# Kernel optimization log

Measured on AMD Instinct MI355X. Metric: run time of the kernel, lower is better.

Reference implementation:

```python
import jax, jax.numpy as jnp
import numpy as np

B, V, R, C, UNITS = 16, 10000, 8, 64, 64


def setup_inputs() -> dict:
    key = jax.random.key(0)
    k1, k2, k3 = jax.random.split(key, 3)
    nodes = jax.random.normal(k1, (B, V, C), dtype=jnp.float32)
    mapping = jax.random.randint(k2, (B, V, R), -1, V, dtype=jnp.int32)
    kernel = jax.random.normal(k3, (R * C, UNITS), dtype=jnp.float32) * 0.02
    bias = jnp.zeros((UNITS,), dtype=jnp.float32)
    return {"nodes": nodes, "mapping": mapping, "kernel": kernel, "bias": bias}


def reference(nodes, mapping, kernel, bias):
    # nodes: [B, V, C], mapping: [B, V, R] int32 in [-1, V)
    b, v, r = mapping.shape
    c = nodes.shape[-1]
    idx = jnp.clip(mapping, 0, v - 1)                       # safe gather indices
    batch_idx = jnp.arange(b, dtype=jnp.int32)[:, None, None]
    gathered = nodes[batch_idx, idx]                        # [B, V, R, C]
    valid = (mapping >= 0)[..., None]                       # -1 -> zero (scatter_nd default)
    cols = jnp.where(valid, gathered, jnp.zeros((), nodes.dtype))
    cols = cols.reshape(b, v, r * c)                        # [B, V, R*C]
    out = jnp.einsum("bvf,fu->bvu", cols, kernel) + bias    # dense + bias
    return jax.nn.relu(out)
```

## Files before the change

### kernel.cpp

```cpp
#include <hip/hip_runtime.h>
#include <hip/hip_fp16.h>


#define Bn 16
#define Vn 10000
#define Rn 8
#define Cn 64
#define Un 64

#define LOSCALE 2048.0f
#define LOINV   (1.0f/2048.0f)

typedef _Float16      f16x8   __attribute__((ext_vector_type(8)));
typedef __fp16        fp16x2  __attribute__((ext_vector_type(2)));
typedef float         f32x16  __attribute__((ext_vector_type(16)));
typedef unsigned int  u32x4   __attribute__((ext_vector_type(4)));
typedef unsigned short us8    __attribute__((ext_vector_type(8)));

__device__ __forceinline__ unsigned short f16b(_Float16 h) {
    return __builtin_bit_cast(unsigned short, h);
}

__device__ __forceinline__ unsigned int cvt2w(float a0, float a1) {
    const fp16x2 p = __builtin_amdgcn_cvt_pkrtz(a0, a1);
    return __builtin_bit_cast(unsigned int, p);
}
__device__ __forceinline__ _Float16 loh(unsigned int w) {
    return __builtin_bit_cast(_Float16, (unsigned short)(w & 0xffff));
}
__device__ __forceinline__ _Float16 hih(unsigned int w) {
    return __builtin_bit_cast(_Float16, (unsigned short)(w >> 16));
}

#define LDS_LO 65536

__global__ __launch_bounds__(512, 2)
void graphconv_kernel(const float* __restrict__ nodes,
                      const int* __restrict__ mapping,
                      const float* __restrict__ kern,
                      const float* __restrict__ bias,
                      float* __restrict__ out) {
    extern __shared__ unsigned char lds[];
    const int tid  = threadIdx.x;
    const int lane = tid & 63;
    const int w    = tid >> 6;
    const int g    = blockIdx.x;
    const int b    = g & 15;
    const int v0   = (g >> 4) << 8;

    const int row = lane & 31;
    const int grp = lane >> 5;
    const int v   = v0 + w * 32 + row;
    const bool vok = v < Vn;

    int4 m03 = make_int4(-1, -1, -1, -1), m47 = make_int4(-1, -1, -1, -1);
    if (vok) {
        const int4* mp4 = (const int4*)(mapping + ((size_t)b * Vn + v) * Rn);
        m03 = mp4[0];
        m47 = mp4[1];
    }

    #pragma unroll
    for (int it = 0; it < 8; ++it) {
        const int gg = it * 512 + tid;
        const int f  = gg >> 6;
        const int l  = gg & 63;
        const int nt = f >> 5;
        const int kt = f & 31;
        const int n  = nt * 32 + (l & 31);
        const int kb = kt * 16 + ((l >> 5) << 3);
        us8 hh, ll;
        #pragma unroll
        for (int j = 0; j < 8; ++j) {
            const float x = kern[(kb + j) * Un + n];
            const _Float16 h  = (_Float16)x;
            const _Float16 lo = (_Float16)((x - (float)h) * LOSCALE);
            hh[j] = f16b(h);
            ll[j] = f16b(lo);
        }
        *(us8*)(lds + (size_t)f * 1024 + (size_t)l * 16)          = hh;
        *(us8*)(lds + LDS_LO + (size_t)f * 1024 + (size_t)l * 16) = ll;
    }
    __syncthreads();

    int mv[8];
    mv[0] = m03.x; mv[1] = m03.y; mv[2] = m03.z; mv[3] = m03.w;
    mv[4] = m47.x; mv[5] = m47.y; mv[6] = m47.z; mv[7] = m47.w;

    f32x16 am0 = {0,0,0,0,0,0,0,0,0,0,0,0,0,0,0,0};
    f32x16 am1 = {0,0,0,0,0,0,0,0,0,0,0,0,0,0,0,0};
    f32x16 ac0 = {0,0,0,0,0,0,0,0,0,0,0,0,0,0,0,0};
    f32x16 ac1 = {0,0,0,0,0,0,0,0,0,0,0,0,0,0,0,0};

    #pragma unroll
    for (int r = 0; r < Rn; ++r) {
        const int mi   = mv[r];
        const int idxc = (mi >= 0) ? mi : 0;
        const unsigned int keep = (mi >= 0) ? 0xffffffffu : 0u;
        const float* src = nodes + ((size_t)b * Vn + idxc) * Cn;
        f16x8 ah[4], al[4];
        #pragma unroll
        for (int kk = 0; kk < 4; ++kk) {
            const int cb = kk * 16 + grp * 8;
            const float4 xa = *(const float4*)(src + cb);
            const float4 xb = *(const float4*)(src + cb + 4);
            u32x4 hw, lw;
            hw[0] = cvt2w(xa.x, xa.y); hw[1] = cvt2w(xa.z, xa.w);
            hw[2] = cvt2w(xb.x, xb.y); hw[3] = cvt2w(xb.z, xb.w);
            lw[0] = cvt2w((xa.x - (float)loh(hw[0])) * LOSCALE,
                          (xa.y - (float)hih(hw[0])) * LOSCALE);
            lw[1] = cvt2w((xa.z - (float)loh(hw[1])) * LOSCALE,
                          (xa.w - (float)hih(hw[1])) * LOSCALE);
            lw[2] = cvt2w((xb.x - (float)loh(hw[2])) * LOSCALE,
                          (xb.y - (float)hih(hw[2])) * LOSCALE);
            lw[3] = cvt2w((xb.z - (float)loh(hw[3])) * LOSCALE,
                          (xb.w - (float)hih(hw[3])) * LOSCALE);
            #pragma unroll
            for (int q = 0; q < 4; ++q) { hw[q] &= keep; lw[q] &= keep; }
            ah[kk] = __builtin_bit_cast(f16x8, hw);
            al[kk] = __builtin_bit_cast(f16x8, lw);
        }
        #pragma unroll
        for (int kk = 0; kk < 4; ++kk) {
            const int kt = r * 4 + kk;
            const size_t fb0 = (size_t)(kt)      * 1024 + (size_t)lane * 16;
            const size_t fb1 = (size_t)(32 + kt) * 1024 + (size_t)lane * 16;
            const f16x8 bh0 = __builtin_bit_cast(f16x8, *(const us8*)(lds + fb0));
            const f16x8 bl0 = __builtin_bit_cast(f16x8, *(const us8*)(lds + LDS_LO + fb0));
            const f16x8 bh1 = __builtin_bit_cast(f16x8, *(const us8*)(lds + fb1));
            const f16x8 bl1 = __builtin_bit_cast(f16x8, *(const us8*)(lds + LDS_LO + fb1));
            am0 = __builtin_amdgcn_mfma_f32_32x32x16_f16(ah[kk], bh0, am0, 0, 0, 0);
            ac0 = __builtin_amdgcn_mfma_f32_32x32x16_f16(al[kk], bh0, ac0, 0, 0, 0);
            ac0 = __builtin_amdgcn_mfma_f32_32x32x16_f16(ah[kk], bl0, ac0, 0, 0, 0);
            am1 = __builtin_amdgcn_mfma_f32_32x32x16_f16(ah[kk], bh1, am1, 0, 0, 0);
            ac1 = __builtin_amdgcn_mfma_f32_32x32x16_f16(al[kk], bh1, ac1, 0, 0, 0);
            ac1 = __builtin_amdgcn_mfma_f32_32x32x16_f16(ah[kk], bl1, ac1, 0, 0, 0);
        }
    }

    const int n0    = lane & 31;
    const float bv0 = bias[n0];
    const float bv1 = bias[32 + n0];
    const int rbase = v0 + w * 32 + 4 * grp;
    #pragma unroll
    for (int q = 0; q < 16; ++q) {
        const int vv = rbase + (q & 3) + 8 * (q >> 2);
        if (vv < Vn) {
            float* o = out + ((size_t)b * Vn + vv) * Un;
            const float x0 = am0[q] + ac0[q] * LOINV + bv0;
            const float x1 = am1[q] + ac1[q] * LOINV + bv1;
            __builtin_nontemporal_store(x0 > 0.f ? x0 : 0.f, o + n0);
            __builtin_nontemporal_store(x1 > 0.f ? x1 : 0.f, o + 32 + n0);
        }
    }
}

extern "C" void kernel_launch(void* const* d_in, const int* in_sizes, int n_in,
                              void* d_out, int out_size, void* d_ws, size_t ws_size,
                              hipStream_t stream) {
    (void)in_sizes; (void)n_in; (void)out_size; (void)d_ws; (void)ws_size;
    const float* nodes   = (const float*)d_in[0];
    const int*   mapping = (const int*)d_in[1];
    const float* kern    = (const float*)d_in[2];
    const float* bias    = (const float*)d_in[3];
    float* out = (float*)d_out;

    static const int lds_bytes = 131072;
    (void)hipFuncSetAttribute(reinterpret_cast<const void*>(&graphconv_kernel),
                              hipFuncAttributeMaxDynamicSharedMemorySize, lds_bytes);
    hipLaunchKernelGGL(graphconv_kernel, dim3(16 * 40), dim3(512), lds_bytes, stream,
                       nodes, mapping, kern, bias, out);
}
```

Before: 156.0 us.

## Prepack split-fp16 weights in a separate kernel and prefetch next gather row

Adds a small prepack kernel that converts the weight matrix to hi/lo fp16 MFMA fragments once into workspace, so each block does a straight 128KB copy into LDS instead of strided global reads plus conversion. The main loop also software-pipelines the neighbour gathers by loading region r+1's row while converting and multiplying region r. This costs one extra launch and more registers for the prefetch buffers, which may pressure occupancy at 512 threads with 2 blocks per CU. A fallback path keeps the old behaviour when no workspace is given.

```diff
diff --git a/kernel.cpp b/kernel.cpp
--- a/kernel.cpp
+++ b/kernel.cpp
@@ -20,7 +20,6 @@
 __device__ __forceinline__ unsigned short f16b(_Float16 h) {
     return __builtin_bit_cast(unsigned short, h);
 }
-
 __device__ __forceinline__ unsigned int cvt2w(float a0, float a1) {
     const fp16x2 p = __builtin_amdgcn_cvt_pkrtz(a0, a1);
     return __builtin_bit_cast(unsigned int, p);
@@ -34,11 +33,35 @@
 
 #define LDS_LO 65536
 
+__global__ __launch_bounds__(256)
+void prepack_b(const float* __restrict__ kern, unsigned char* __restrict__ ws) {
+    const int g  = blockIdx.x * 256 + threadIdx.x;
+    const int f  = g >> 6;
+    const int l  = g & 63;
+    const int nt = f >> 5;
+    const int kt = f & 31;
+    const int n  = nt * 32 + (l & 31);
+    const int kb = kt * 16 + ((l >> 5) << 3);
+    us8 hh, ll;
+    #pragma unroll
+    for (int j = 0; j < 8; ++j) {
+        const float x = kern[(kb + j) * Un + n];
+        const _Float16 h  = (_Float16)x;
+        const _Float16 lo = (_Float16)((x - (float)h) * LOSCALE);
+        hh[j] = f16b(h);
+        ll[j] = f16b(lo);
+    }
+    *(us8*)(ws + (size_t)g * 16)          = hh;
+    *(us8*)(ws + LDS_LO + (size_t)g * 16) = ll;
+}
+
+template <bool FAST>
 __global__ __launch_bounds__(512, 2)
 void graphconv_kernel(const float* __restrict__ nodes,
                       const int* __restrict__ mapping,
                       const float* __restrict__ kern,
                       const float* __restrict__ bias,
+                      const unsigned char* __restrict__ ws,
                       float* __restrict__ out) {
     extern __shared__ unsigned char lds[];
     const int tid  = threadIdx.x;
@@ -60,50 +83,76 @@
         m47 = mp4[1];
     }
 
-    #pragma unroll
-    for (int it = 0; it < 8; ++it) {
-        const int gg = it * 512 + tid;
-        const int f  = gg >> 6;
-        const int l  = gg & 63;
-        const int nt = f >> 5;
-        const int kt = f & 31;
-        const int n  = nt * 32 + (l & 31);
-        const int kb = kt * 16 + ((l >> 5) << 3);
-        us8 hh, ll;
-        #pragma unroll
-        for (int j = 0; j < 8; ++j) {
-            const float x = kern[(kb + j) * Un + n];
-            const _Float16 h  = (_Float16)x;
-            const _Float16 lo = (_Float16)((x - (float)h) * LOSCALE);
-            hh[j] = f16b(h);
-            ll[j] = f16b(lo);
-        }
-        *(us8*)(lds + (size_t)f * 1024 + (size_t)l * 16)          = hh;
-        *(us8*)(lds + LDS_LO + (size_t)f * 1024 + (size_t)l * 16) = ll;
+    if (FAST) {
+        const uint4* srcw = (const uint4*)ws;
+        uint4* dstw = (uint4*)lds;
+        #pragma unroll
+        for (int i = 0; i < 16; ++i) dstw[i * 512 + tid] = srcw[i * 512 + tid];
+    } else {
+        #pragma unroll
+        for (int it = 0; it < 8; ++it) {
+            const int gg = it * 512 + tid;
+            const int f  = gg >> 6;
+            const int l  = gg & 63;
+            const int nt = f >> 5;
+            const int kt = f & 31;
+            const int n  = nt * 32 + (l & 31);
+            const int kb = kt * 16 + ((l >> 5) << 3);
+            us8 hh, ll;
+            #pragma unroll
+            for (int j = 0; j < 8; ++j) {
+                const float x = kern[(kb + j) * Un + n];
+                const _Float16 h  = (_Float16)x;
+                const _Float16 lo = (_Float16)((x - (float)h) * LOSCALE);
+                hh[j] = f16b(h);
+                ll[j] = f16b(lo);
+            }
+            *(us8*)(lds + (size_t)gg * 16)          = hh;
+            *(us8*)(lds + LDS_LO + (size_t)gg * 16) = ll;
+        }
     }
     __syncthreads();
 
     int mv[8];
     mv[0] = m03.x; mv[1] = m03.y; mv[2] = m03.z; mv[3] = m03.w;
     mv[4] = m47.x; mv[5] = m47.y; mv[6] = m47.z; mv[7] = m47.w;
+
+    const float* srcs[8];
+    unsigned int keep[8];
+    #pragma unroll
+    for (int r = 0; r < Rn; ++r) {
+        const int mi = mv[r];
+        keep[r] = (mi >= 0) ? 0xffffffffu : 0u;
+        srcs[r] = nodes + ((size_t)b * Vn + (mi >= 0 ? mi : 0)) * Cn + grp * 8;
+    }
 
     f32x16 am0 = {0,0,0,0,0,0,0,0,0,0,0,0,0,0,0,0};
     f32x16 am1 = {0,0,0,0,0,0,0,0,0,0,0,0,0,0,0,0};
     f32x16 ac0 = {0,0,0,0,0,0,0,0,0,0,0,0,0,0,0,0};
     f32x16 ac1 = {0,0,0,0,0,0,0,0,0,0,0,0,0,0,0,0};
 
+    float4 ca[4], cb4[4], na[4], nb4[4];
+    #pragma unroll
+    for (int kk = 0; kk < 4; ++kk) {
+        ca[kk]  = *(const float4*)(srcs[0] + kk * 16);
+        cb4[kk] = *(const float4*)(srcs[0] + kk * 16 + 4);
+    }
+
     #pragma unroll
     for (int r = 0; r < Rn; ++r) {
-        const int mi   = mv[r];
-        const int idxc = (mi >= 0) ? mi : 0;
-        const unsigned int keep = (mi >= 0) ? 0xffffffffu : 0u;
-        const float* src = nodes + ((size_t)b * Vn + idxc) * Cn;
+        if (r + 1 < Rn) {
+            #pragma unroll
+            for (int kk = 0; kk < 4; ++kk) {
+                na[kk]  = *(const float4*)(srcs[r + 1] + kk * 16);
+                nb4[kk] = *(const float4*)(srcs[r + 1] + kk * 16 + 4);
+            }
+        }
+        const unsigned int kp = keep[r];
         f16x8 ah[4], al[4];
         #pragma unroll
         for (int kk = 0; kk < 4; ++kk) {
-            const int cb = kk * 16 + grp * 8;
-            const float4 xa = *(const float4*)(src + cb);
-            const float4 xb = *(const float4*)(src + cb + 4);
+            const float4 xa = ca[kk];
+            const float4 xb = cb4[kk];
             u32x4 hw, lw;
             hw[0] = cvt2w(xa.x, xa.y); hw[1] = cvt2w(xa.z, xa.w);
             hw[2] = cvt2w(xb.x, xb.y); hw[3] = cvt2w(xb.z, xb.w);
@@ -116,7 +165,7 @@
             lw[3] = cvt2w((xb.z - (float)loh(hw[3])) * LOSCALE,
                           (xb.w - (float)hih(hw[3])) * LOSCALE);
             #pragma unroll
-            for (int q = 0; q < 4; ++q) { hw[q] &= keep; lw[q] &= keep; }
+            for (int q = 0; q < 4; ++q) { hw[q] &= kp; lw[q] &= kp; }
             ah[kk] = __builtin_bit_cast(f16x8, hw);
             al[kk] = __builtin_bit_cast(f16x8, lw);
         }
@@ -136,6 +185,10 @@
             ac1 = __builtin_amdgcn_mfma_f32_32x32x16_f16(al[kk], bh1, ac1, 0, 0, 0);
             ac1 = __builtin_amdgcn_mfma_f32_32x32x16_f16(ah[kk], bl1, ac1, 0, 0, 0);
         }
+        if (r + 1 < Rn) {
+            #pragma unroll
+            for (int kk = 0; kk < 4; ++kk) { ca[kk] = na[kk]; cb4[kk] = nb4[kk]; }
+        }
     }
 
     const int n0    = lane & 31;
@@ -158,16 +211,31 @@
 extern "C" void kernel_launch(void* const* d_in, const int* in_sizes, int n_in,
                               void* d_out, int out_size, void* d_ws, size_t ws_size,
                               hipStream_t stream) {
-    (void)in_sizes; (void)n_in; (void)out_size; (void)d_ws; (void)ws_size;
+    (void)in_sizes; (void)n_in; (void)out_size;
     const float* nodes   = (const float*)d_in[0];
     const int*   mapping = (const int*)d_in[1];
     const float* kern    = (const float*)d_in[2];
     const float* bias    = (const float*)d_in[3];
     float* out = (float*)d_out;
+    unsigned char* ws = (unsigned char*)d_ws;
 
     static const int lds_bytes = 131072;
-    (void)hipFuncSetAttribute(reinterpret_cast<const void*>(&graphconv_kernel),
-                              hipFuncAttributeMaxDynamicSharedMemorySize, lds_bytes);
-    hipLaunchKernelGGL(graphconv_kernel, dim3(16 * 40), dim3(512), lds_bytes, stream,
-                       nodes, mapping, kern, bias, out);
-}
+    const bool fast = (ws != nullptr) && (ws_size >= 131072);
+
+    if (fast) {
+        hipLaunchKernelGGL(prepack_b, dim3(16), dim3(256), 0, stream, kern, ws);
+        (void)hipFuncSetAttribute(
+            reinterpret_cast<const void*>(&graphconv_kernel<true>),
+            hipFuncAttributeMaxDynamicSharedMemorySize, lds_bytes);
+        hipLaunchKernelGGL(HIP_KERNEL_NAME(graphconv_kernel<true>),
+                           dim3(16 * 40), dim3(512), lds_bytes, stream,
+                           nodes, mapping, kern, bias, ws, out);
+    } else {
+        (void)hipFuncSetAttribute(
+            reinterpret_cast<const void*>(&graphconv_kernel<false>),
+            hipFuncAttributeMaxDynamicSharedMemorySize, lds_bytes);
+        hipLaunchKernelGGL(HIP_KERNEL_NAME(graphconv_kernel<false>),
+                           dim3(16 * 40), dim3(512), lds_bytes, stream,
+                           nodes, mapping, kern, bias, ws, out);
+    }
+}
```

Measured after the change: 156.0 us. About the same (+0.0%).
